# Kernel optimization log

Hardware: AMD Instinct MI355X
Metric: run time of the kernel (lower is better)

## Reference

```python
import jax, jax.numpy as jnp
import numpy as np

B = 8192; N = 50; NUM_NODES = 200000; NUM_EDGES = 1000000
FEAT = 64; EFEAT = 4; TD = 16; D = 64


def setup_inputs() -> dict:
    key = jax.random.key(0)
    ks = jax.random.split(key, 32)
    p = lambda i, shape: jax.random.normal(ks[i], shape, jnp.float32) * 0.05
    inp = {}
    nf = jax.random.normal(ks[0], (NUM_NODES, FEAT), jnp.float32)
    skills = jax.random.randint(ks[1], (NUM_NODES,), 0, 100).astype(jnp.float32)
    inp['node_raw_features'] = nf.at[:, 0].set(skills)  # col 0 = skill id
    inp['edge_raw_features'] = jax.random.normal(ks[2], (NUM_EDGES, EFEAT), jnp.float32)
    inp['src_node_ids'] = jax.random.randint(ks[3], (B,), 0, NUM_NODES)
    inp['dst_node_ids'] = jax.random.randint(ks[4], (B,), 0, NUM_NODES)
    inp['node_interact_times'] = jax.random.uniform(ks[5], (B,), jnp.float32, 0.0, 1e4)
    inp['src_neighbor_node_ids'] = jax.random.randint(ks[6], (B, N), 0, NUM_NODES)
    inp['src_neighbor_edge_ids'] = jax.random.randint(ks[7], (B, N), 0, NUM_EDGES)
    inp['src_neighbor_times'] = jax.random.uniform(ks[8], (B, N), jnp.float32, 0.0, 1e4)
    inp['dst_neighbor_node_ids'] = jax.random.randint(ks[9], (B, N), 0, NUM_NODES)
    inp['dst_neighbor_edge_ids'] = jax.random.randint(ks[10], (B, N), 0, NUM_EDGES)
    inp['dst_neighbor_times'] = jax.random.uniform(ks[11], (B, N), jnp.float32, 0.0, 1e4)
    # projection layers
    inp['W_feat'] = p(12, (FEAT, D)); inp['b_feat'] = p(13, (D,))
    inp['W_edge'] = p(14, (1, D));    inp['b_edge'] = p(15, (D,))
    inp['W_time'] = p(16, (TD, D));   inp['b_time'] = p(17, (D,))
    inp['W_struct'] = p(18, (1, D));  inp['b_struct'] = p(19, (D,))
    inp['W_out'] = p(20, (D, D));     inp['b_out'] = p(21, (D,))
    # time encoder (cos(w*dt + b), trainable Linear(1, TD) as in TGN TimeEncoder)
    inp['time_w'] = p(22, (TD,)); inp['time_b'] = p(23, (TD,))
    # src / dst GRUs (PyTorch layout: W_ih [3H,E], W_hh [3H,H])
    inp['src_W_ih'] = p(24, (3 * D, D)); inp['src_W_hh'] = p(25, (3 * D, D))
    inp['src_b_ih'] = p(26, (3 * D,));   inp['src_b_hh'] = p(27, (3 * D,))
    inp['dst_W_ih'] = p(28, (3 * D, D)); inp['dst_W_hh'] = p(29, (3 * D, D))
    inp['dst_b_ih'] = p(30, (3 * D,));   inp['dst_b_hh'] = p(31, (3 * D,))
    return inp


def _lin(x, W, b):
    return x @ W + b


def _gru_last_hidden(x, W_ih, W_hh, b_ih, b_hh):
    # x: [B, T, E] -> final hidden state [B, H] (PyTorch GRU equations)
    Bb, _, _ = x.shape
    H = W_hh.shape[1]

    def step(h, xt):
        gi = xt @ W_ih.T + b_ih            # [B, 3H]
        gh = h @ W_hh.T + b_hh             # [B, 3H]
        ir, iz, inn = jnp.split(gi, 3, axis=-1)
        hr, hz, hn = jnp.split(gh, 3, axis=-1)
        r = jax.nn.sigmoid(ir + hr)
        z = jax.nn.sigmoid(iz + hz)
        n = jnp.tanh(inn + r * hn)
        h_new = (1.0 - z) * n + z * h
        return h_new, None

    h0 = jnp.zeros((Bb, H), x.dtype)
    hT, _ = jax.lax.scan(step, h0, jnp.swapaxes(x, 0, 1))
    return hT


def reference(node_raw_features, edge_raw_features, src_node_ids, dst_node_ids,
              node_interact_times, src_neighbor_node_ids, src_neighbor_edge_ids,
              src_neighbor_times, dst_neighbor_node_ids, dst_neighbor_edge_ids,
              dst_neighbor_times, W_feat, b_feat, W_edge, b_edge, W_time, b_time,
              W_struct, b_struct, W_out, b_out, time_w, time_b,
              src_W_ih, src_W_hh, src_b_ih, src_b_hh,
              dst_W_ih, dst_W_hh, dst_b_ih, dst_b_hh):
    t = node_interact_times
    # append the query interaction itself (edge id 0) -> [B, N+1]
    src_nids = jnp.concatenate([src_neighbor_node_ids, src_node_ids[:, None]], 1)
    src_eids = jnp.concatenate([src_neighbor_edge_ids, jnp.zeros_like(src_node_ids)[:, None]], 1)
    src_ts = jnp.concatenate([src_neighbor_times, t[:, None]], 1)
    dst_nids = jnp.concatenate([dst_neighbor_node_ids, dst_node_ids[:, None]], 1)
    dst_eids = jnp.concatenate([dst_neighbor_edge_ids, jnp.zeros_like(dst_node_ids)[:, None]], 1)
    dst_ts = jnp.concatenate([dst_neighbor_times, t[:, None]], 1)

    # co-occurrence features [B, N, 1]
    co_src = (src_neighbor_node_ids == dst_node_ids[:, None]).astype(jnp.float32)[..., None]
    co_dst = (dst_neighbor_node_ids == src_node_ids[:, None]).astype(jnp.float32)[..., None]
    # skill match features [B, N, 1]
    src_skill = node_raw_features[src_nids][:, :-1, 0].astype(jnp.int32)
    dst_skill = node_raw_features[dst_nids][:, -1, 0].astype(jnp.int32)[:, None]
    skill_f = (src_skill == dst_skill).astype(jnp.float32)[..., None]

    src_struct = _lin(co_src, W_struct, b_struct)
    dst_struct = _lin(co_dst, W_struct, b_struct)
    skill_struct = _lin(skill_f, W_struct, b_struct)

    def get_feats(nids, eids, ts):
        node_f = _lin(node_raw_features[nids], W_feat, b_feat)        # [B,N+1,D]
        delta = t[:, None] - ts                                       # dual-decay ablation: delta times
        tenc = jnp.cos(delta[..., None] * time_w + time_b)            # [B,N+1,TD]
        time_f = _lin(tenc, W_time, b_time)                           # [B,N+1,D]
        edge_f = _lin(edge_raw_features[eids][..., :1], W_edge, b_edge)
        return node_f, edge_f, time_f

    sn, se, st = get_feats(src_nids, src_eids, src_ts)
    dn, de, dt = get_feats(dst_nids, dst_eids, dst_ts)
    src_feats = sn + se + st
    dst_feats = dn + de + dt

    src_emb = _gru_last_hidden(src_feats[:, :-1] + skill_struct + src_struct,
                               src_W_ih, src_W_hh, src_b_ih, src_b_hh) + (se + st)[:, -1]
    dst_emb = _gru_last_hidden((de + dt)[:, :-1] + dst_struct,
                               dst_W_ih, dst_W_hh, dst_b_ih, dst_b_hh) + dst_feats[:, -1]

    return _lin(src_emb, W_out, b_out), _lin(dst_emb, W_out, b_out)
```

## Files before the change

kernel.cpp:

```cpp
#include <hip/hip_runtime.h>
#include <stdint.h>

#define BB 8192
#define NN 50

typedef _Float16 half8 __attribute__((ext_vector_type(8)));
typedef float floatx4 __attribute__((ext_vector_type(4)));

union FragU { uint4 u; half8 h; };
static __device__ __forceinline__ half8 u2h(uint4 u) { FragU f; f.u = u; return f.h; }

static __device__ __forceinline__ uint32_t pk2u(float a, float b) {
    auto p = __builtin_amdgcn_cvt_pkrtz(a, b);
    uint32_t u; __builtin_memcpy(&u, &p, 4); return u;
}

#define MFMA(A, B, C) __builtin_amdgcn_mfma_f32_16x16x32_f16((A), (B), (C), 0, 0, 0)

static __device__ __forceinline__ float frcp(float x) {
#if __has_builtin(__builtin_amdgcn_rcpf)
    return __builtin_amdgcn_rcpf(x);
#else
    return 1.0f / x;
#endif
}
static __device__ __forceinline__ float fexp2(float x) {
#if __has_builtin(__builtin_amdgcn_exp2f)
    return __builtin_amdgcn_exp2f(x);
#else
    return __expf(0.69314718056f * x);
#endif
}

static __device__ __forceinline__ void bar_lds() {
    asm volatile("s_waitcnt lgkmcnt(0)" ::: "memory");
    __builtin_amdgcn_s_barrier();
}

__global__ __launch_bounds__(128, 2)
void dygkt11(const float* __restrict__ nodef, const float* __restrict__ edgef,
             const int* __restrict__ src_ids, const int* __restrict__ dst_ids,
             const float* __restrict__ times,
             const int* __restrict__ s_nids, const int* __restrict__ s_eids,
             const float* __restrict__ s_ts,
             const int* __restrict__ d_nids, const int* __restrict__ d_eids,
             const float* __restrict__ d_ts,
             const float* __restrict__ W_feat, const float* __restrict__ b_feat,
             const float* __restrict__ W_edge, const float* __restrict__ b_edge,
             const float* __restrict__ W_time, const float* __restrict__ b_time,
             const float* __restrict__ W_str,  const float* __restrict__ b_str,
             const float* __restrict__ W_out,  const float* __restrict__ b_out,
             const float* __restrict__ time_w, const float* __restrict__ time_b,
             const float* __restrict__ sWih, const float* __restrict__ sWhh,
             const float* __restrict__ sbih, const float* __restrict__ sbhh,
             const float* __restrict__ dWih, const float* __restrict__ dWhh,
             const float* __restrict__ dbih, const float* __restrict__ dbhh,
             float* __restrict__ out)
{
    __shared__ uint4 wfA[8][64];
    __shared__ uint4 woA[8][64];
    __shared__ __align__(16) _Float16 xls[2][16 * 72];
    __shared__ __align__(16) _Float16 hls[2][16 * 72];

    const int tid = threadIdx.x, w = tid >> 6, lane = tid & 63;
    const int g = lane >> 4, i16 = lane & 15;
    const bool is_src = blockIdx.x < 512;
    const int b = (int)(blockIdx.x & 511) * 16 + i16;

    const float SRZ = -1.44269504089f;
    const float SN  =  2.88539008178f;
    const floatx4 z4 = {0, 0, 0, 0};

    for (int q = tid; q < 512; q += 128) {
        int l = q & 63, tt = q >> 6;
        int kh = tt >> 2, mt = tt & 3, gg = l >> 4, ii = l & 15;
        float v[8], u[8];
        #pragma unroll
        for (int j = 0; j < 8; ++j) {
            int k = 32 * kh + 8 * gg + j, m = 16 * mt + ii;
            v[j] = W_feat[k * 64 + m];
            u[j] = W_out[k * 64 + m];
        }
        wfA[tt][l] = make_uint4(pk2u(v[0],v[1]), pk2u(v[2],v[3]), pk2u(v[4],v[5]), pk2u(v[6],v[7]));
        woA[tt][l] = make_uint4(pk2u(u[0],u[1]), pk2u(u[2],u[3]), pk2u(u[4],u[5]), pk2u(u[6],u[7]));
    }
    for (int q = tid; q < 16 * 72 / 2; q += 128) ((uint32_t*)hls[0])[q] = 0u;

    const float* WI = is_src ? sWih : dWih;
    const float* WH = is_src ? sWhh : dWhh;
    uint4 wih[6][2], whh[6][2];
    #pragma unroll
    for (int gt = 0; gt < 3; ++gt) {
        const float s = (gt == 2) ? SN : SRZ;
        #pragma unroll
        for (int tq = 0; tq < 2; ++tq)
            #pragma unroll
            for (int kh = 0; kh < 2; ++kh) {
                int row = 64 * gt + 16 * (2 * w + tq) + i16;
                const float* p = WI + (size_t)row * 64 + 32 * kh + 8 * g;
                float4 a = *(const float4*)p, c = *(const float4*)(p + 4);
                wih[gt * 2 + tq][kh] = make_uint4(pk2u(s*a.x,s*a.y), pk2u(s*a.z,s*a.w),
                                                  pk2u(s*c.x,s*c.y), pk2u(s*c.z,s*c.w));
                const float* qq = WH + (size_t)row * 64 + 32 * kh + 8 * g;
                float4 e = *(const float4*)qq, f = *(const float4*)(qq + 4);
                whh[gt * 2 + tq][kh] = make_uint4(pk2u(s*e.x,s*e.y), pk2u(s*e.z,s*e.w),
                                                  pk2u(s*f.x,s*f.y), pk2u(s*f.z,s*f.w));
            }
    }

    uint4 wtA[2];
    #pragma unroll
    for (int tq = 0; tq < 2; ++tq) {
        int mt = 2 * w + tq;
        float v[8];
        #pragma unroll
        for (int j = 0; j < 8; ++j) {
            int k = 8 * g + j, dim = 16 * mt + i16;
            float x = 0.0f;
            if (k < 16)       x = W_time[k * 64 + dim];
            else if (k == 16) x = W_edge[dim];
            else if (k == 17) x = W_str[dim];
            else if (k == 18) x = b_edge[dim] + b_time[dim];
            else if (k == 19) x = is_src ? (b_feat[dim] + 2.0f * b_str[dim]) : b_str[dim];
            else if (k == 20) x = b_feat[dim];
            v[j] = x;
        }
        wtA[tq] = make_uint4(pk2u(v[0],v[1]), pk2u(v[2],v[3]), pk2u(v[4],v[5]), pk2u(v[6],v[7]));
    }

    const float* BI = is_src ? sbih : dbih;
    const float* BH = is_src ? sbhh : dbhh;
    floatx4 brz[4], bin[2], bhn[2];
    #pragma unroll
    for (int gz = 0; gz < 2; ++gz)
        #pragma unroll
        for (int tq = 0; tq < 2; ++tq) {
            int r0 = 64 * gz + 16 * (2 * w + tq) + 4 * g;
            floatx4 v;
            #pragma unroll
            for (int r = 0; r < 4; ++r) v[r] = SRZ * (BI[r0 + r] + BH[r0 + r]);
            brz[gz * 2 + tq] = v;
        }
    #pragma unroll
    for (int tq = 0; tq < 2; ++tq) {
        int r0 = 128 + 16 * (2 * w + tq) + 4 * g;
        floatx4 vi, vh;
        #pragma unroll
        for (int r = 0; r < 4; ++r) { vi[r] = SN * BI[r0 + r]; vh[r] = SN * BH[r0 + r]; }
        bin[tq] = vi; bhn[tq] = vh;
    }

    const int* pn = (is_src ? s_nids : d_nids) + (size_t)b * NN;
    const int* pe = (is_src ? s_eids : d_eids) + (size_t)b * NN;
    const float* pt = (is_src ? s_ts : d_ts) + (size_t)b * NN;
    const float tqL = times[b];
    const int didL = dst_ids[b];
    const int oid = is_src ? didL : src_ids[b];
    const float dskill = is_src ? nodef[(size_t)didL * 64] : 0.0f;
    float twc[8], tbc[8];
    #pragma unroll
    for (int j = 0; j < 8; ++j) {
        int k = 8 * (g & 1) + j;
        twc[j] = time_w[k]; tbc[j] = time_b[k];
    }

    __syncthreads();

    int nidC = pn[0], eidC = pe[0];
    float tsC = pt[0];
    float e0C = edgef[4 * (size_t)eidC];
    float nskC = 0.0f;
    float4 nfa = {0,0,0,0}, nfb = {0,0,0,0}, nfc = {0,0,0,0}, nfd = {0,0,0,0};
    if (is_src) {
        const float* rp = nodef + (size_t)nidC * 64 + 8 * g;
        nfa = *(const float4*)rp;        nfb = *(const float4*)(rp + 4);
        nfc = *(const float4*)(rp + 32); nfd = *(const float4*)(rp + 36);
        nskC = nodef[(size_t)nidC * 64];
    }

    floatx4 hM[2] = {z4, z4};
    int cur = 0;

    for (int t = 0; t < NN; ++t) {
        int nidN = 0, eidN = 0; float tsN = 0.0f;
        if (t + 1 < NN) { nidN = pn[t + 1]; eidN = pe[t + 1]; tsN = pt[t + 1]; }

        float sf = ((nidC == oid) ? 1.0f : 0.0f) +
                   ((is_src && nskC == dskill) ? 1.0f : 0.0f);
        float delta = tqL - tsC;
        uint4 tb4;
        if (g < 2) {
            float cv[8];
            #pragma unroll
            for (int j = 0; j < 8; ++j) cv[j] = __cosf(delta * twc[j] + tbc[j]);
            tb4 = make_uint4(pk2u(cv[0],cv[1]), pk2u(cv[2],cv[3]), pk2u(cv[4],cv[5]), pk2u(cv[6],cv[7]));
        } else if (g == 2) {
            tb4 = make_uint4(pk2u(e0C, sf), pk2u(1.0f, 1.0f), 0u, 0u);
        } else {
            tb4 = make_uint4(0u, 0u, 0u, 0u);
        }
        half8 tB = u2h(tb4);

        if (is_src) {
            uint4 nf0 = make_uint4(pk2u(nfa.x,nfa.y), pk2u(nfa.z,nfa.w), pk2u(nfb.x,nfb.y), pk2u(nfb.z,nfb.w));
            uint4 nf1 = make_uint4(pk2u(nfc.x,nfc.y), pk2u(nfc.z,nfc.w), pk2u(nfd.x,nfd.y), pk2u(nfd.z,nfd.w));
            half8 nB0 = u2h(nf0), nB1 = u2h(nf1);
            #pragma unroll
            for (int tq = 0; tq < 2; ++tq) {
                int mt = 2 * w + tq;
                floatx4 a = MFMA(u2h(wfA[mt][lane]), nB0, z4);
                a = MFMA(u2h(wfA[4 + mt][lane]), nB1, a);
                floatx4 xacc = MFMA(u2h(wtA[tq]), tB, a);
                *(uint2*)&xls[cur][i16 * 72 + 32 * w + 16 * tq + 4 * g] =
                    make_uint2(pk2u(xacc[0], xacc[1]), pk2u(xacc[2], xacc[3]));
            }
        } else {
            #pragma unroll
            for (int tq = 0; tq < 2; ++tq) {
                floatx4 xacc = MFMA(u2h(wtA[tq]), tB, z4);
                *(uint2*)&xls[cur][i16 * 72 + 32 * w + 16 * tq + 4 * g] =
                    make_uint2(pk2u(xacc[0], xacc[1]), pk2u(xacc[2], xacc[3]));
            }
        }

        float e0N = 0.0f, nskN = 0.0f;
        float4 na = {0,0,0,0}, nb = {0,0,0,0}, nc = {0,0,0,0}, nd = {0,0,0,0};
        if (t + 1 < NN) {
            e0N = edgef[4 * (size_t)eidN];
            if (is_src) {
                const float* rp = nodef + (size_t)nidN * 64 + 8 * g;
                na = *(const float4*)rp;        nb = *(const float4*)(rp + 4);
                nc = *(const float4*)(rp + 32); nd = *(const float4*)(rp + 36);
                nskN = nodef[(size_t)nidN * 64];
            }
        }

        bar_lds();

        half8 xB0 = u2h(*(const uint4*)&xls[cur][i16 * 72 + 8 * g]);
        half8 xB1 = u2h(*(const uint4*)&xls[cur][i16 * 72 + 32 + 8 * g]);
        half8 hB0 = u2h(*(const uint4*)&hls[cur][i16 * 72 + 8 * g]);
        half8 hB1 = u2h(*(const uint4*)&hls[cur][i16 * 72 + 32 + 8 * g]);

        floatx4 rg[2], zg[2], ia[2], ha[2];
        #pragma unroll
        for (int tq = 0; tq < 2; ++tq) {
            floatx4 a = MFMA(u2h(wih[tq][0]), xB0, brz[tq]);
            a = MFMA(u2h(wih[tq][1]), xB1, a);
            a = MFMA(u2h(whh[tq][0]), hB0, a);
            rg[tq] = MFMA(u2h(whh[tq][1]), hB1, a);
        }
        #pragma unroll
        for (int tq = 0; tq < 2; ++tq) {
            floatx4 a = MFMA(u2h(wih[2 + tq][0]), xB0, brz[2 + tq]);
            a = MFMA(u2h(wih[2 + tq][1]), xB1, a);
            a = MFMA(u2h(whh[2 + tq][0]), hB0, a);
            zg[tq] = MFMA(u2h(whh[2 + tq][1]), hB1, a);
        }
        #pragma unroll
        for (int tq = 0; tq < 2; ++tq) {
            floatx4 a = MFMA(u2h(wih[4 + tq][0]), xB0, bin[tq]);
            ia[tq] = MFMA(u2h(wih[4 + tq][1]), xB1, a);
            floatx4 c = MFMA(u2h(whh[4 + tq][0]), hB0, bhn[tq]);
            ha[tq] = MFMA(u2h(whh[4 + tq][1]), hB1, c);
        }

        #pragma unroll
        for (int tq = 0; tq < 2; ++tq)
            #pragma unroll
            for (int r = 0; r < 4; ++r) {
                float rr = frcp(1.0f + fexp2(rg[tq][r]));
                float zz = frcp(1.0f + fexp2(zg[tq][r]));
                float nn = 1.0f - 2.0f * frcp(fexp2(ia[tq][r] + rr * ha[tq][r]) + 1.0f);
                hM[tq][r] = nn + zz * (hM[tq][r] - nn);
            }

        #pragma unroll
        for (int tq = 0; tq < 2; ++tq)
            *(uint2*)&hls[cur ^ 1][i16 * 72 + 32 * w + 16 * tq + 4 * g] =
                make_uint2(pk2u(hM[tq][0], hM[tq][1]), pk2u(hM[tq][2], hM[tq][3]));

        cur ^= 1;
        nidC = nidN; eidC = eidN; tsC = tsN; e0C = e0N; nskC = nskN;
        nfa = na; nfb = nb; nfc = nc; nfd = nd;
    }

    float e00 = edgef[0];
    uint4 tt4;
    if (g < 2) {
        float cv[8];
        #pragma unroll
        for (int j = 0; j < 8; ++j) cv[j] = __cosf(tbc[j]);
        tt4 = make_uint4(pk2u(cv[0],cv[1]), pk2u(cv[2],cv[3]), pk2u(cv[4],cv[5]), pk2u(cv[6],cv[7]));
    } else if (g == 2) {
        tt4 = make_uint4(pk2u(e00, 0.0f), pk2u(1.0f, 0.0f), pk2u(is_src ? 0.0f : 1.0f, 0.0f), 0u);
    } else {
        tt4 = make_uint4(0u, 0u, 0u, 0u);
    }
    half8 tT = u2h(tt4);

    floatx4 tacc[2];
    #pragma unroll
    for (int tq = 0; tq < 2; ++tq) tacc[tq] = MFMA(u2h(wtA[tq]), tT, z4);
    if (!is_src) {
        const float* rp = nodef + (size_t)didL * 64 + 8 * g;
        float4 da = *(const float4*)rp,        db = *(const float4*)(rp + 4);
        float4 dc = *(const float4*)(rp + 32), dd = *(const float4*)(rp + 36);
        uint4 d0 = make_uint4(pk2u(da.x,da.y), pk2u(da.z,da.w), pk2u(db.x,db.y), pk2u(db.z,db.w));
        uint4 d1 = make_uint4(pk2u(dc.x,dc.y), pk2u(dc.z,dc.w), pk2u(dd.x,dd.y), pk2u(dd.z,dd.w));
        #pragma unroll
        for (int tq = 0; tq < 2; ++tq) {
            int mt = 2 * w + tq;
            tacc[tq] = MFMA(u2h(wfA[mt][lane]), u2h(d0), tacc[tq]);
            tacc[tq] = MFMA(u2h(wfA[4 + mt][lane]), u2h(d1), tacc[tq]);
        }
    }

    #pragma unroll
    for (int tq = 0; tq < 2; ++tq) {
        floatx4 e = hM[tq] + tacc[tq];
        *(uint2*)&xls[0][i16 * 72 + 32 * w + 16 * tq + 4 * g] =
            make_uint2(pk2u(e[0], e[1]), pk2u(e[2], e[3]));
    }
    bar_lds();
    half8 eB0 = u2h(*(const uint4*)&xls[0][i16 * 72 + 8 * g]);
    half8 eB1 = u2h(*(const uint4*)&xls[0][i16 * 72 + 32 + 8 * g]);

    const size_t obase = (is_src ? 0 : (size_t)BB * 64) + (size_t)b * 64;
    #pragma unroll
    for (int tq = 0; tq < 2; ++tq) {
        int mt = 2 * w + tq;
        floatx4 bo;
        #pragma unroll
        for (int r = 0; r < 4; ++r) bo[r] = b_out[16 * mt + 4 * g + r];
        floatx4 o = MFMA(u2h(woA[mt][lane]), eB0, bo);
        o = MFMA(u2h(woA[4 + mt][lane]), eB1, o);
        #pragma unroll
        for (int r = 0; r < 4; ++r)
            out[obase + 16 * mt + 4 * g + r] = o[r];
    }
}

extern "C" void kernel_launch(void* const* d_in, const int* in_sizes, int n_in,
                              void* d_out, int out_size, void* d_ws, size_t ws_size,
                              hipStream_t stream) {
    (void)in_sizes; (void)n_in; (void)d_ws; (void)ws_size; (void)out_size;
    const float* nodef  = (const float*)d_in[0];
    const float* edgef  = (const float*)d_in[1];
    const int*   srcid  = (const int*)  d_in[2];
    const int*   dstid  = (const int*)  d_in[3];
    const float* times  = (const float*)d_in[4];
    const int*   s_nids = (const int*)  d_in[5];
    const int*   s_eids = (const int*)  d_in[6];
    const float* s_ts   = (const float*)d_in[7];
    const int*   d_nids = (const int*)  d_in[8];
    const int*   d_eids = (const int*)  d_in[9];
    const float* d_ts   = (const float*)d_in[10];
    const float* W_feat = (const float*)d_in[11];
    const float* b_feat = (const float*)d_in[12];
    const float* W_edge = (const float*)d_in[13];
    const float* b_edge = (const float*)d_in[14];
    const float* W_time = (const float*)d_in[15];
    const float* b_time = (const float*)d_in[16];
    const float* W_str  = (const float*)d_in[17];
    const float* b_str  = (const float*)d_in[18];
    const float* W_out  = (const float*)d_in[19];
    const float* b_out  = (const float*)d_in[20];
    const float* time_w = (const float*)d_in[21];
    const float* time_b = (const float*)d_in[22];
    const float* sWih   = (const float*)d_in[23];
    const float* sWhh   = (const float*)d_in[24];
    const float* sbih   = (const float*)d_in[25];
    const float* sbhh   = (const float*)d_in[26];
    const float* dWih   = (const float*)d_in[27];
    const float* dWhh   = (const float*)d_in[28];
    const float* dbih   = (const float*)d_in[29];
    const float* dbhh   = (const float*)d_in[30];

    dim3 grid(1024), block(128);
    dygkt11<<<grid, block, 0, stream>>>(
        nodef, edgef, srcid, dstid, times,
        s_nids, s_eids, s_ts, d_nids, d_eids, d_ts,
        W_feat, b_feat, W_edge, b_edge, W_time, b_time,
        W_str, b_str, W_out, b_out, time_w, time_b,
        sWih, sWhh, sbih, sbhh, dWih, dWhh, dbih, dbhh,
        (float*)d_out);
}
```

Measured before the change: 241.9 us.

## Halve batch rows per block, double grid, keep W_out fragments in registers

Each block now processes 8 batch rows instead of 16 and the grid is doubled, with src and dst blocks interleaved by block index parity. The 16-wide MFMA columns now hold duplicated rows, and only lanes 0-7 write to LDS and global memory. The W_out LDS tile is dropped and its fragments are loaded into registers just before the output projection, which shrinks shared memory. The aim is more resident blocks to hide the latency of the serial 50-step GRU recurrence, at the cost of doubling total MFMA work and weight-staging overhead.

```diff
diff --git a/kernel.cpp b/kernel.cpp
--- a/kernel.cpp
+++ b/kernel.cpp
@@ -38,7 +38,7 @@
 }
 
 __global__ __launch_bounds__(128, 2)
-void dygkt11(const float* __restrict__ nodef, const float* __restrict__ edgef,
+void dygkt12(const float* __restrict__ nodef, const float* __restrict__ edgef,
              const int* __restrict__ src_ids, const int* __restrict__ dst_ids,
              const float* __restrict__ times,
              const int* __restrict__ s_nids, const int* __restrict__ s_eids,
@@ -58,14 +58,13 @@
              float* __restrict__ out)
 {
     __shared__ uint4 wfA[8][64];
-    __shared__ uint4 woA[8][64];
-    __shared__ __align__(16) _Float16 xls[2][16 * 72];
-    __shared__ __align__(16) _Float16 hls[2][16 * 72];
+    __shared__ __align__(16) _Float16 xls[2][8 * 72];
+    __shared__ __align__(16) _Float16 hls[2][8 * 72];
 
     const int tid = threadIdx.x, w = tid >> 6, lane = tid & 63;
-    const int g = lane >> 4, i16 = lane & 15;
-    const bool is_src = blockIdx.x < 512;
-    const int b = (int)(blockIdx.x & 511) * 16 + i16;
+    const int g = lane >> 4, i16 = lane & 15, i8 = lane & 7;
+    const bool is_src = (blockIdx.x & 1) == 0;
+    const int b = (int)(blockIdx.x >> 1) * 8 + i8;
 
     const float SRZ = -1.44269504089f;
     const float SN  =  2.88539008178f;
@@ -74,17 +73,13 @@
     for (int q = tid; q < 512; q += 128) {
         int l = q & 63, tt = q >> 6;
         int kh = tt >> 2, mt = tt & 3, gg = l >> 4, ii = l & 15;
-        float v[8], u[8];
-        #pragma unroll
-        for (int j = 0; j < 8; ++j) {
-            int k = 32 * kh + 8 * gg + j, m = 16 * mt + ii;
-            v[j] = W_feat[k * 64 + m];
-            u[j] = W_out[k * 64 + m];
-        }
+        float v[8];
+        #pragma unroll
+        for (int j = 0; j < 8; ++j)
+            v[j] = W_feat[(32 * kh + 8 * gg + j) * 64 + 16 * mt + ii];
         wfA[tt][l] = make_uint4(pk2u(v[0],v[1]), pk2u(v[2],v[3]), pk2u(v[4],v[5]), pk2u(v[6],v[7]));
-        woA[tt][l] = make_uint4(pk2u(u[0],u[1]), pk2u(u[2],u[3]), pk2u(u[4],u[5]), pk2u(u[6],u[7]));
-    }
-    for (int q = tid; q < 16 * 72 / 2; q += 128) ((uint32_t*)hls[0])[q] = 0u;
+    }
+    for (int q = tid; q < 8 * 72 / 2; q += 128) ((uint32_t*)hls[0])[q] = 0u;
 
     const float* WI = is_src ? sWih : dWih;
     const float* WH = is_src ? sWhh : dWhh;
@@ -211,15 +206,17 @@
                 floatx4 a = MFMA(u2h(wfA[mt][lane]), nB0, z4);
                 a = MFMA(u2h(wfA[4 + mt][lane]), nB1, a);
                 floatx4 xacc = MFMA(u2h(wtA[tq]), tB, a);
-                *(uint2*)&xls[cur][i16 * 72 + 32 * w + 16 * tq + 4 * g] =
-                    make_uint2(pk2u(xacc[0], xacc[1]), pk2u(xacc[2], xacc[3]));
+                if (i16 < 8)
+                    *(uint2*)&xls[cur][i16 * 72 + 32 * w + 16 * tq + 4 * g] =
+                        make_uint2(pk2u(xacc[0], xacc[1]), pk2u(xacc[2], xacc[3]));
             }
         } else {
             #pragma unroll
             for (int tq = 0; tq < 2; ++tq) {
                 floatx4 xacc = MFMA(u2h(wtA[tq]), tB, z4);
-                *(uint2*)&xls[cur][i16 * 72 + 32 * w + 16 * tq + 4 * g] =
-                    make_uint2(pk2u(xacc[0], xacc[1]), pk2u(xacc[2], xacc[3]));
+                if (i16 < 8)
+                    *(uint2*)&xls[cur][i16 * 72 + 32 * w + 16 * tq + 4 * g] =
+                        make_uint2(pk2u(xacc[0], xacc[1]), pk2u(xacc[2], xacc[3]));
             }
         }
 
@@ -237,10 +234,10 @@
 
         bar_lds();
 
-        half8 xB0 = u2h(*(const uint4*)&xls[cur][i16 * 72 + 8 * g]);
-        half8 xB1 = u2h(*(const uint4*)&xls[cur][i16 * 72 + 32 + 8 * g]);
-        half8 hB0 = u2h(*(const uint4*)&hls[cur][i16 * 72 + 8 * g]);
-        half8 hB1 = u2h(*(const uint4*)&hls[cur][i16 * 72 + 32 + 8 * g]);
+        half8 xB0 = u2h(*(const uint4*)&xls[cur][i8 * 72 + 8 * g]);
+        half8 xB1 = u2h(*(const uint4*)&xls[cur][i8 * 72 + 32 + 8 * g]);
+        half8 hB0 = u2h(*(const uint4*)&hls[cur][i8 * 72 + 8 * g]);
+        half8 hB1 = u2h(*(const uint4*)&hls[cur][i8 * 72 + 32 + 8 * g]);
 
         floatx4 rg[2], zg[2], ia[2], ha[2];
         #pragma unroll
@@ -275,10 +272,12 @@
                 hM[tq][r] = nn + zz * (hM[tq][r] - nn);
             }
 
-        #pragma unroll
-        for (int tq = 0; tq < 2; ++tq)
-            *(uint2*)&hls[cur ^ 1][i16 * 72 + 32 * w + 16 * tq + 4 * g] =
-                make_uint2(pk2u(hM[tq][0], hM[tq][1]), pk2u(hM[tq][2], hM[tq][3]));
+        if (i16 < 8) {
+            #pragma unroll
+            for (int tq = 0; tq < 2; ++tq)
+                *(uint2*)&hls[cur ^ 1][i16 * 72 + 32 * w + 16 * tq + 4 * g] =
+                    make_uint2(pk2u(hM[tq][0], hM[tq][1]), pk2u(hM[tq][2], hM[tq][3]));
+        }
 
         cur ^= 1;
         nidC = nidN; eidC = eidN; tsC = tsN; e0C = e0N; nskC = nskN;
@@ -316,15 +315,29 @@
         }
     }
 
-    #pragma unroll
-    for (int tq = 0; tq < 2; ++tq) {
-        floatx4 e = hM[tq] + tacc[tq];
-        *(uint2*)&xls[0][i16 * 72 + 32 * w + 16 * tq + 4 * g] =
-            make_uint2(pk2u(e[0], e[1]), pk2u(e[2], e[3]));
+    uint4 wo[2][2];
+    #pragma unroll
+    for (int tq = 0; tq < 2; ++tq)
+        #pragma unroll
+        for (int kh = 0; kh < 2; ++kh) {
+            float v[8];
+            #pragma unroll
+            for (int j = 0; j < 8; ++j)
+                v[j] = W_out[(32 * kh + 8 * g + j) * 64 + 16 * (2 * w + tq) + i16];
+            wo[tq][kh] = make_uint4(pk2u(v[0],v[1]), pk2u(v[2],v[3]), pk2u(v[4],v[5]), pk2u(v[6],v[7]));
+        }
+
+    if (i16 < 8) {
+        #pragma unroll
+        for (int tq = 0; tq < 2; ++tq) {
+            floatx4 e = hM[tq] + tacc[tq];
+            *(uint2*)&xls[0][i16 * 72 + 32 * w + 16 * tq + 4 * g] =
+                make_uint2(pk2u(e[0], e[1]), pk2u(e[2], e[3]));
+        }
     }
     bar_lds();
-    half8 eB0 = u2h(*(const uint4*)&xls[0][i16 * 72 + 8 * g]);
-    half8 eB1 = u2h(*(const uint4*)&xls[0][i16 * 72 + 32 + 8 * g]);
+    half8 eB0 = u2h(*(const uint4*)&xls[0][i8 * 72 + 8 * g]);
+    half8 eB1 = u2h(*(const uint4*)&xls[0][i8 * 72 + 32 + 8 * g]);
 
     const size_t obase = (is_src ? 0 : (size_t)BB * 64) + (size_t)b * 64;
     #pragma unroll
@@ -333,11 +346,13 @@
         floatx4 bo;
         #pragma unroll
         for (int r = 0; r < 4; ++r) bo[r] = b_out[16 * mt + 4 * g + r];
-        floatx4 o = MFMA(u2h(woA[mt][lane]), eB0, bo);
-        o = MFMA(u2h(woA[4 + mt][lane]), eB1, o);
-        #pragma unroll
-        for (int r = 0; r < 4; ++r)
-            out[obase + 16 * mt + 4 * g + r] = o[r];
+        floatx4 o = MFMA(u2h(wo[tq][0]), eB0, bo);
+        o = MFMA(u2h(wo[tq][1]), eB1, o);
+        if (i16 < 8) {
+            #pragma unroll
+            for (int r = 0; r < 4; ++r)
+                out[obase + 16 * mt + 4 * g + r] = o[r];
+        }
     }
 }
 
@@ -377,8 +392,8 @@
     const float* dbih   = (const float*)d_in[29];
     const float* dbhh   = (const float*)d_in[30];
 
-    dim3 grid(1024), block(128);
-    dygkt11<<<grid, block, 0, stream>>>(
+    dim3 grid(2048), block(128);
+    dygkt12<<<grid, block, 0, stream>>>(
         nodef, edgef, srcid, dstid, times,
         s_nids, s_eids, s_ts, d_nids, d_eids, d_ts,
         W_feat, b_feat, W_edge, b_edge, W_time, b_time,
```

After: 398.0 us. 64.5% more time.
